# Kernel optimization log

Measured on AMD Instinct MI355X. Metric: run time of the kernel, lower is better.

The kernel has to match this reference:

```python
import jax, jax.numpy as jnp
import numpy as np
from jax import lax

F = 88  # piano-roll feature dim, hard-coded in the original module


def setup_inputs() -> dict:
    key = jax.random.key(0)
    k1, k2, k3 = jax.random.split(key, 3)
    N, T, window = 128, 2048, 64
    x = jax.random.normal(k1, (N, T, F), dtype=jnp.float32)
    W = jax.random.normal(k2, (F, window * F), dtype=jnp.float32) * 0.02
    b = jax.random.normal(k3, (F,), dtype=jnp.float32) * 0.02
    return {"x": x, "W": W, "b": b}


def reference(x, W, b):
    # x: (N, T, F). Original: for each t, flatten x[:, t-window:t] (time-major),
    # LEFT-zero-pad to window*F, apply Linear(W, b). Exclusive of frame t, so the
    # effective receptive field for output t is frames [t-window, t-1] -> a
    # strictly-causal conv over time with kernel size `window`.
    N, T, _ = x.shape
    window = W.shape[1] // F
    # Left-pad `window` zero frames; window for output t is xp[:, t:t+window],
    # which equals x[:, t-window:t] with zeros filling missing early frames
    # (matching the original's left-side zero concat after flattening).
    xp = jnp.pad(x, ((0, 0), (window, 0), (0, 0)))  # (N, T+window, F)
    # Flattened index layout is tau*F + f, so W reshapes to (out=F, tau, f).
    K = W.reshape(F, window, F).transpose(1, 2, 0)  # WIO: (window, F_in, F_out)
    out = lax.conv_general_dilated(
        xp, K, window_strides=(1,), padding="VALID",
        dimension_numbers=("NWC", "WIO", "NWC"),
    )  # (N, T+1, F); valid starts 0..T, we need starts 0..T-1
    out = out[:, :T] + b  # (N, T, F)
    return (out, out)
```

## Files before the change

kernel.cpp:

```cpp
#include <hip/hip_runtime.h>
#include <hip/hip_bf16.h>

#define NBATCH 128
#define TLEN   2048
#define FDIM   88
#define WIN    64
#define TT     128
#define FRAMES (TT + WIN)
#define LSTR   100
#define BSLICE (18 * 512)
#define BCHUNK 1152

typedef __attribute__((ext_vector_type(8))) short short8;
typedef __attribute__((ext_vector_type(4))) short short4v;
typedef __attribute__((ext_vector_type(4))) float floatx4;

static __device__ __forceinline__ unsigned short f2bf(float f) {
    union { float f; unsigned int u; } a; a.f = f;
    unsigned int u = a.u;
    u += 0x7fffu + ((u >> 16) & 1u);
    return (unsigned short)(u >> 16);
}

static __device__ __forceinline__ void gload_lds16(const unsigned short* g, unsigned short* l) {
    __builtin_amdgcn_global_load_lds(
        (const __attribute__((address_space(1))) unsigned int*)g,
        (__attribute__((address_space(3))) unsigned int*)l, 16, 0, 0);
}

__global__ void prep_w(const float* __restrict__ W, unsigned short* __restrict__ Wt) {
    int idx = blockIdx.x * blockDim.x + threadIdx.x;
    if (idx >= WIN * BSLICE) return;
    int j    = idx & 7;
    int lane = (idx >> 3) & 63;
    int rest = idx >> 9;
    int nt   = rest % 6;
    int kkt  = rest / 6;
    int kk   = kkt % 3;
    int tau  = kkt / 3;
    int n = nt * 16 + (lane & 15);
    int k = kk * 32 + (lane >> 4) * 8 + j;
    float v = 0.f;
    if (n < FDIM && k < FDIM) v = W[n * (WIN * FDIM) + tau * FDIM + k];
    Wt[idx] = f2bf(v);
}

__global__ __launch_bounds__(256, 2) void conv_mfma(
    const float* __restrict__ x, const unsigned short* __restrict__ Wt,
    const float* __restrict__ bias, float* __restrict__ out)
{
    __shared__ unsigned short xs[FRAMES * LSTR];
    __shared__ unsigned short bufB[2][BSLICE];

    const int tb  = blockIdx.x;
    const int nb  = blockIdx.y;
    const int t0  = tb * TT;
    const int tid = threadIdx.x;

    for (int c = tid; c < BCHUNK; c += 256)
        gload_lds16(Wt + (size_t)c * 8, &bufB[0][c * 8]);

    const float* xn = x + (size_t)nb * TLEN * FDIM;
    for (int idx = tid; idx < FRAMES * 25; idx += 256) {
        int i = idx / 25;
        int c = idx % 25;
        int g = t0 - WIN + i;
        short4v v = (short4v){0, 0, 0, 0};
        if (c < 22 && g >= 0) {
            float4 f = *((const float4*)(xn + (size_t)g * FDIM) + c);
            v.x = (short)f2bf(f.x); v.y = (short)f2bf(f.y);
            v.z = (short)f2bf(f.z); v.w = (short)f2bf(f.w);
        }
        *(short4v*)&xs[i * LSTR + c * 4] = v;
    }
    __syncthreads();

    const int wave = tid >> 6;
    const int lane = tid & 63;
    const int m    = lane & 15;
    const int quad = lane >> 4;
    const int wrow = (wave >> 1) * 64;
    const int wcol = (wave & 1) * 48;
    const int nt0  = (wave & 1) * 3;

    floatx4 acc[4][3] = {};

    const int a_base = (wrow + m) * LSTR + quad * 8;

    for (int tau = 0; tau < WIN; ++tau) {
        if (tau + 1 < WIN) {
            const unsigned short* src = Wt + (size_t)(tau + 1) * BSLICE;
            unsigned short* dst = bufB[(tau + 1) & 1];
            for (int c = tid; c < BCHUNK; c += 256)
                gload_lds16(src + c * 8, dst + c * 8);
        }
        const unsigned short* bp = bufB[tau & 1];
        const int a_tau = a_base + tau * LSTR;
        #pragma unroll
        for (int kk = 0; kk < 3; ++kk) {
            short8 bf[3];
            #pragma unroll
            for (int n_t = 0; n_t < 3; ++n_t)
                bf[n_t] = *(const short8*)(bp + (kk * 6 + nt0 + n_t) * 512 + lane * 8);
            short8 af[4];
            #pragma unroll
            for (int m_t = 0; m_t < 4; ++m_t)
                af[m_t] = *(const short8*)&xs[a_tau + m_t * 16 * LSTR + kk * 32];
            __builtin_amdgcn_s_setprio(1);
            #pragma unroll
            for (int m_t = 0; m_t < 4; ++m_t)
                #pragma unroll
                for (int n_t = 0; n_t < 3; ++n_t)
                    acc[m_t][n_t] = __builtin_amdgcn_mfma_f32_16x16x32_bf16(
                        af[m_t], bf[n_t], acc[m_t][n_t], 0, 0, 0);
            __builtin_amdgcn_s_setprio(0);
        }
        __syncthreads();
    }

    float bv[3];
    #pragma unroll
    for (int n_t = 0; n_t < 3; ++n_t) {
        int c = wcol + n_t * 16 + m;
        bv[n_t] = (c < FDIM) ? bias[c] : 0.f;
    }
    const size_t half = (size_t)NBATCH * TLEN * FDIM;
    #pragma unroll
    for (int n_t = 0; n_t < 3; ++n_t) {
        int c = wcol + n_t * 16 + m;
        if (c >= FDIM) continue;
        #pragma unroll
        for (int m_t = 0; m_t < 4; ++m_t) {
            #pragma unroll
            for (int reg = 0; reg < 4; ++reg) {
                int tr = wrow + m_t * 16 + quad * 4 + reg;
                size_t off = ((size_t)nb * TLEN + (t0 + tr)) * FDIM + c;
                float v = acc[m_t][n_t][reg] + bv[n_t];
                out[off] = v;
                out[half + off] = v;
            }
        }
    }
}

extern "C" void kernel_launch(void* const* d_in, const int* in_sizes, int n_in,
                              void* d_out, int out_size, void* d_ws, size_t ws_size,
                              hipStream_t stream) {
    const float* x = (const float*)d_in[0];
    const float* W = (const float*)d_in[1];
    const float* b = (const float*)d_in[2];
    float* out = (float*)d_out;
    unsigned short* Wt = (unsigned short*)d_ws;

    prep_w<<<(WIN * BSLICE + 255) / 256, 256, 0, stream>>>(W, Wt);
    dim3 grid(TLEN / TT, NBATCH);
    conv_mfma<<<grid, 256, 0, stream>>>(x, Wt, b, out);
}
```

Before: 563.5 us.

## Load weight fragments directly to registers and double time tile per block

Drops the LDS double-buffer for weight slices. Each wave now loads its B fragments straight from global memory into registers, with a software-pipelined ping-pong between kk steps. The time tile grows to 256 frames, so each wave holds 8x3 accumulators, which improves reuse of weight loads across more output rows. In exchange it raises register pressure, halves the grid size, and puts weight loads on L2/global latency instead of LDS.

```diff
diff --git a/kernel.cpp b/kernel.cpp
--- a/kernel.cpp
+++ b/kernel.cpp
@@ -5,11 +5,10 @@
 #define TLEN   2048
 #define FDIM   88
 #define WIN    64
-#define TT     128
+#define TT     256
 #define FRAMES (TT + WIN)
 #define LSTR   100
 #define BSLICE (18 * 512)
-#define BCHUNK 1152
 
 typedef __attribute__((ext_vector_type(8))) short short8;
 typedef __attribute__((ext_vector_type(4))) short short4v;
@@ -20,12 +19,6 @@
     unsigned int u = a.u;
     u += 0x7fffu + ((u >> 16) & 1u);
     return (unsigned short)(u >> 16);
-}
-
-static __device__ __forceinline__ void gload_lds16(const unsigned short* g, unsigned short* l) {
-    __builtin_amdgcn_global_load_lds(
-        (const __attribute__((address_space(1))) unsigned int*)g,
-        (__attribute__((address_space(3))) unsigned int*)l, 16, 0, 0);
 }
 
 __global__ void prep_w(const float* __restrict__ W, unsigned short* __restrict__ Wt) {
@@ -45,20 +38,51 @@
     Wt[idx] = f2bf(v);
 }
 
+static __device__ __forceinline__ void load_bfrags(short8* dst, const unsigned short* __restrict__ Wt,
+                                                   int tau, int kk, int nt0, int lane) {
+    const unsigned short* p = Wt + (size_t)tau * BSLICE + (size_t)((kk * 6 + nt0) * 512) + lane * 8;
+    #pragma unroll
+    for (int n_t = 0; n_t < 3; ++n_t)
+        dst[n_t] = *(const short8*)(p + n_t * 512);
+}
+
+static __device__ __forceinline__ void mfma_step(floatx4 acc[8][3], const short8* bf,
+                                                 const unsigned short* xs, int a_tau, int kk) {
+    short8 af[8];
+    #pragma unroll
+    for (int m_t = 0; m_t < 8; ++m_t)
+        af[m_t] = *(const short8*)&xs[a_tau + m_t * 16 * LSTR + kk * 32];
+    __builtin_amdgcn_s_setprio(1);
+    #pragma unroll
+    for (int m_t = 0; m_t < 8; ++m_t)
+        #pragma unroll
+        for (int n_t = 0; n_t < 3; ++n_t)
+            acc[m_t][n_t] = __builtin_amdgcn_mfma_f32_16x16x32_bf16(
+                af[m_t], bf[n_t], acc[m_t][n_t], 0, 0, 0);
+    __builtin_amdgcn_s_setprio(0);
+}
+
 __global__ __launch_bounds__(256, 2) void conv_mfma(
     const float* __restrict__ x, const unsigned short* __restrict__ Wt,
     const float* __restrict__ bias, float* __restrict__ out)
 {
     __shared__ unsigned short xs[FRAMES * LSTR];
-    __shared__ unsigned short bufB[2][BSLICE];
 
     const int tb  = blockIdx.x;
     const int nb  = blockIdx.y;
     const int t0  = tb * TT;
     const int tid = threadIdx.x;
 
-    for (int c = tid; c < BCHUNK; c += 256)
-        gload_lds16(Wt + (size_t)c * 8, &bufB[0][c * 8]);
+    const int wave = tid >> 6;
+    const int lane = tid & 63;
+    const int m    = lane & 15;
+    const int quad = lane >> 4;
+    const int wrow = (wave >> 1) * 128;
+    const int wcol = (wave & 1) * 48;
+    const int nt0  = (wave & 1) * 3;
+
+    short8 bA[3], bB[3];
+    load_bfrags(bA, Wt, 0, 0, nt0, lane);
 
     const float* xn = x + (size_t)nb * TLEN * FDIM;
     for (int idx = tid; idx < FRAMES * 25; idx += 256) {
@@ -75,47 +99,27 @@
     }
     __syncthreads();
 
-    const int wave = tid >> 6;
-    const int lane = tid & 63;
-    const int m    = lane & 15;
-    const int quad = lane >> 4;
-    const int wrow = (wave >> 1) * 64;
-    const int wcol = (wave & 1) * 48;
-    const int nt0  = (wave & 1) * 3;
-
-    floatx4 acc[4][3] = {};
-
+    floatx4 acc[8][3] = {};
     const int a_base = (wrow + m) * LSTR + quad * 8;
 
-    for (int tau = 0; tau < WIN; ++tau) {
-        if (tau + 1 < WIN) {
-            const unsigned short* src = Wt + (size_t)(tau + 1) * BSLICE;
-            unsigned short* dst = bufB[(tau + 1) & 1];
-            for (int c = tid; c < BCHUNK; c += 256)
-                gload_lds16(src + c * 8, dst + c * 8);
-        }
-        const unsigned short* bp = bufB[tau & 1];
-        const int a_tau = a_base + tau * LSTR;
-        #pragma unroll
-        for (int kk = 0; kk < 3; ++kk) {
-            short8 bf[3];
-            #pragma unroll
-            for (int n_t = 0; n_t < 3; ++n_t)
-                bf[n_t] = *(const short8*)(bp + (kk * 6 + nt0 + n_t) * 512 + lane * 8);
-            short8 af[4];
-            #pragma unroll
-            for (int m_t = 0; m_t < 4; ++m_t)
-                af[m_t] = *(const short8*)&xs[a_tau + m_t * 16 * LSTR + kk * 32];
-            __builtin_amdgcn_s_setprio(1);
-            #pragma unroll
-            for (int m_t = 0; m_t < 4; ++m_t)
-                #pragma unroll
-                for (int n_t = 0; n_t < 3; ++n_t)
-                    acc[m_t][n_t] = __builtin_amdgcn_mfma_f32_16x16x32_bf16(
-                        af[m_t], bf[n_t], acc[m_t][n_t], 0, 0, 0);
-            __builtin_amdgcn_s_setprio(0);
-        }
-        __syncthreads();
+    for (int tau = 0; tau < WIN; tau += 2) {
+        const int at0 = a_base + tau * LSTR;
+        const int at1 = at0 + LSTR;
+        __builtin_amdgcn_s_barrier();
+        load_bfrags(bB, Wt, tau, 1, nt0, lane);
+        mfma_step(acc, bA, xs, at0, 0);
+        load_bfrags(bA, Wt, tau, 2, nt0, lane);
+        mfma_step(acc, bB, xs, at0, 1);
+        load_bfrags(bB, Wt, tau + 1, 0, nt0, lane);
+        mfma_step(acc, bA, xs, at0, 2);
+        __builtin_amdgcn_s_barrier();
+        load_bfrags(bA, Wt, tau + 1, 1, nt0, lane);
+        mfma_step(acc, bB, xs, at1, 0);
+        load_bfrags(bB, Wt, tau + 1, 2, nt0, lane);
+        mfma_step(acc, bA, xs, at1, 1);
+        if (tau + 2 < WIN)
+            load_bfrags(bA, Wt, tau + 2, 0, nt0, lane);
+        mfma_step(acc, bB, xs, at1, 2);
     }
 
     float bv[3];
@@ -130,7 +134,7 @@
         int c = wcol + n_t * 16 + m;
         if (c >= FDIM) continue;
         #pragma unroll
-        for (int m_t = 0; m_t < 4; ++m_t) {
+        for (int m_t = 0; m_t < 8; ++m_t) {
             #pragma unroll
             for (int reg = 0; reg < 4; ++reg) {
                 int tr = wrow + m_t * 16 + quad * 4 + reg;
```

Result: slower. 936.3 us (+66.1%).
